# Kernel optimization log

Hardware: AMD Instinct MI355X
Metric: run time of the kernel (lower is better)

The kernel has to match this reference:

```python
import jax, jax.numpy as jnp
import numpy as np
import math

N_STFT = 1025
N_MELS = 128
SAMPLE_RATE = 16000
F_MIN = 0.0
F_MAX = 8000.0
MAX_ITER = 20
LR = 0.3
MOMENTUM = 0.9
BATCH = 4
TIME = 1024


def _create_fb_matrix(n_freqs, f_min, f_max, n_mels, sample_rate):
    # Triangular mel filterbank, (n_freqs, n_mels), matching torchaudio's create_fb_matrix.
    all_freqs = np.linspace(0.0, sample_rate // 2, n_freqs)
    m_min = 2595.0 * math.log10(1.0 + f_min / 700.0)
    m_max = 2595.0 * math.log10(1.0 + f_max / 700.0)
    m_pts = np.linspace(m_min, m_max, n_mels + 2)
    f_pts = 700.0 * (10.0 ** (m_pts / 2595.0) - 1.0)
    f_diff = f_pts[1:] - f_pts[:-1]
    slopes = f_pts[None, :] - all_freqs[:, None]  # (n_freqs, n_mels+2)
    down_slopes = -slopes[:, :-2] / f_diff[:-1]
    up_slopes = slopes[:, 2:] / f_diff[1:]
    fb = np.maximum(0.0, np.minimum(down_slopes, up_slopes))
    return jnp.asarray(fb, dtype=jnp.float32)


def setup_inputs() -> dict:
    key = jax.random.key(0)
    k1, k2 = jax.random.split(key)
    melspec = jax.random.uniform(k1, (BATCH, N_MELS, TIME), dtype=jnp.float32)
    # torch.rand initialization of the estimated spectrogram, exposed for determinism
    spec_init = jax.random.uniform(k2, (BATCH, TIME, N_STFT), dtype=jnp.float32)
    fb = _create_fb_matrix(N_STFT, F_MIN, F_MAX, N_MELS, SAMPLE_RATE)
    return {"melspec": melspec, "spec_init": spec_init, "fb": fb}


def reference(melspec, spec_init, fb):
    # melspec: (B, n_mels, T) -> (B, T, n_mels); fb: (n_stft, n_mels)
    mel_t = jnp.swapaxes(melspec, -1, -2)
    b, t, _ = mel_t.shape
    inv = 2.0 / (b * t)  # d(mean over B*T of sum_m diff^2)/d(spec) prefactor

    def step(carry, _):
        spec, buf = carry
        diff = mel_t - jnp.einsum('btf,fm->btm', spec, fb)      # (B,T,M)
        grad = -inv * jnp.einsum('btm,fm->btf', diff, fb)       # (B,T,F)
        buf = MOMENTUM * buf + grad                              # SGD momentum buffer
        spec = jnp.maximum(spec - LR * buf, 0.0)                 # update + clamp(min=0)
        return (spec, buf), None

    init = (spec_init, jnp.zeros_like(spec_init))
    (spec, _), _ = jax.lax.scan(step, init, None, length=MAX_ITER)
    return jnp.swapaxes(spec, -1, -2)  # (B, n_stft, T)
```

## Files before the change

### kernel.cpp

```cpp
#include <hip/hip_runtime.h>

#define N_STFT 1025
#define N_MELS 128
#define BATCH 4
#define TIME 1024
#define MAX_ITER 20

__global__ void imel_prep(const float* __restrict__ fb, int* __restrict__ m0f,
                          float* __restrict__ w0a, float* __restrict__ w1a) {
  const int w = threadIdx.x >> 6, l = threadIdx.x & 63;
  const int f = blockIdx.x * 4 + w;
  if (f >= N_STFT) return;
  const float* row = fb + (size_t)f * N_MELS;
  const unsigned long long mlo = __ballot(row[l] != 0.0f);
  const unsigned long long mhi = __ballot(row[l + 64] != 0.0f);
  if (l == 0) {
    int m0 = mlo ? __builtin_ctzll(mlo)
                 : (mhi ? 64 + __builtin_ctzll(mhi) : 0);
    if (m0 > N_MELS - 2) m0 = N_MELS - 2;
    m0f[f] = m0;
    w0a[f] = row[m0];
    w1a[f] = row[m0 + 1];
  }
}

__global__ __launch_bounds__(512, 8) void imel_main(
    const float* __restrict__ melspec, const float* __restrict__ spec_init,
    const int* __restrict__ m0f, const float* __restrict__ w0a,
    const float* __restrict__ w1a, float* __restrict__ out) {
  __shared__ int   s_Pi[4][4][129];
  __shared__ float s_diff[4][N_MELS];
  __shared__ float s_out[4][1060];

  const int tid = threadIdx.x;
  const int w   = tid >> 6;
  const int l   = tid & 63;
  const int row = w >> 1;
  const int h   = w & 1;
  const int c   = h * 64 + l;
  const int r   = l & 3;
  const int blk = blockIdx.x;
  const int b   = blk >> 8;
  const int t0  = (blk & 255) << 2;
  const int t   = t0 + row;

  const float SCALE = 16777216.0f;
  const float INV_SCALE = 1.0f / 16777216.0f;

  float rs[9], rb[9], rw0[9], rw1[9];
  int rm0[9];

  const float* srow = spec_init + (size_t)(b * TIME + t) * N_STFT;
#pragma unroll
  for (int k = 0; k < 9; ++k) {
    const int f = (c << 3) + k;
    const bool ok = (k < 8) || (c == 127);
    if (ok) {
      rs[k] = srow[f];
      rm0[k] = m0f[f];
      rw0[k] = w0a[f] * SCALE;
      rw1[k] = w1a[f] * SCALE;
    } else {
      rs[k] = 0.f; rm0[k] = 0; rw0[k] = 0.f; rw1[k] = 0.f;
    }
    rb[k] = 0.f;
  }

  const int dr = tid >> 7, dm = tid & 127;
  const float melD = melspec[((size_t)b * N_MELS + dm) * TIME + t0 + dr];

  for (int i = tid; i < 4 * 4 * 129; i += 512) ((int*)s_Pi)[i] = 0;
  __syncthreads();

  const float GRAD_C = (-2.0f / (BATCH * TIME)) * INV_SCALE;

  for (int it = 0; it < MAX_ITER; ++it) {
#pragma unroll
    for (int k = 0; k < 9; ++k) {
      if (k < 8 || c == 127) {
        atomicAdd(&s_Pi[row][r][rm0[k]],     __float2int_rn(rs[k] * rw0[k]));
        atomicAdd(&s_Pi[row][r][rm0[k] + 1], __float2int_rn(rs[k] * rw1[k]));
      }
    }
    __syncthreads();
    {
      const int p = s_Pi[dr][0][dm] + s_Pi[dr][1][dm] +
                    s_Pi[dr][2][dm] + s_Pi[dr][3][dm];
      s_diff[dr][dm] = melD - (float)p * INV_SCALE;
      s_Pi[dr][0][dm] = 0; s_Pi[dr][1][dm] = 0;
      s_Pi[dr][2][dm] = 0; s_Pi[dr][3][dm] = 0;
    }
    __syncthreads();
#pragma unroll
    for (int k = 0; k < 9; ++k) {
      if (k < 8 || c == 127) {
        const float d0 = s_diff[row][rm0[k]];
        const float d1 = s_diff[row][rm0[k] + 1];
        const float g = GRAD_C * (d0 * rw0[k] + d1 * rw1[k]);
        rb[k] = 0.9f * rb[k] + g;
        const float s = rs[k] - 0.3f * rb[k];
        rs[k] = s > 0.f ? s : 0.f;
      }
    }
  }

#pragma unroll
  for (int k = 0; k < 9; ++k) {
    if (k < 8 || c == 127) {
      const int f = (c << 3) + k;
      s_out[row][f + (f >> 5)] = rs[k];
    }
  }
  __syncthreads();

  const int tl = tid & 3;
  const int fg = tid >> 2;
  float* obase = out + (size_t)b * N_STFT * TIME + t0 + tl;
  for (int f = fg; f < N_STFT; f += 128) {
    obase[(size_t)f * TIME] = s_out[tl][f + (f >> 5)];
  }
}

extern "C" void kernel_launch(void* const* d_in, const int* in_sizes, int n_in,
                              void* d_out, int out_size, void* d_ws, size_t ws_size,
                              hipStream_t stream) {
  const float* melspec = (const float*)d_in[0];
  const float* spec_init = (const float*)d_in[1];
  const float* fb = (const float*)d_in[2];
  float* out = (float*)d_out;

  int* m0f = (int*)d_ws;
  float* w0a = (float*)((char*)d_ws + 5120);
  float* w1a = (float*)((char*)d_ws + 10240);

  imel_prep<<<dim3(257), dim3(256), 0, stream>>>(fb, m0f, w0a, w1a);
  imel_main<<<dim3(1024), dim3(512), 0, stream>>>(melspec, spec_init, m0f, w0a, w1a, out);
}
```

Baseline: 134.4 us.

## Assign one wavefront per time row and combine runs before LDS atomics

Each 64-lane wavefront now owns a whole time row, 16 frequency bins per lane, with a private LDS accumulator. That lets the two block-wide __syncthreads per iteration become wave-level barriers. Bins sharing the same mel index are summed in registers before a single atomic, which cuts LDS atomic traffic. The constant melspec part of the gradient is precomputed once per bin. The last frequency bin is carried through unchanged, which relies on its filterbank row being all zero.

```diff
diff --git a/kernel.cpp b/kernel.cpp
--- a/kernel.cpp
+++ b/kernel.cpp
@@ -5,6 +5,8 @@
 #define BATCH 4
 #define TIME 1024
 #define MAX_ITER 20
+
+typedef unsigned int u32;
 
 __global__ void imel_prep(const float* __restrict__ fb, int* __restrict__ m0f,
                           float* __restrict__ w0a, float* __restrict__ w1a) {
@@ -24,99 +26,107 @@
   }
 }
 
-__global__ __launch_bounds__(512, 8) void imel_main(
+__global__ __launch_bounds__(256, 4) void imel_main(
     const float* __restrict__ melspec, const float* __restrict__ spec_init,
     const int* __restrict__ m0f, const float* __restrict__ w0a,
     const float* __restrict__ w1a, float* __restrict__ out) {
-  __shared__ int   s_Pi[4][4][129];
-  __shared__ float s_diff[4][N_MELS];
+  __shared__ u32   s_P[4][N_MELS];
+  __shared__ float s_mel[4][N_MELS];
   __shared__ float s_out[4][1060];
 
   const int tid = threadIdx.x;
   const int w   = tid >> 6;
   const int l   = tid & 63;
-  const int row = w >> 1;
-  const int h   = w & 1;
-  const int c   = h * 64 + l;
-  const int r   = l & 3;
   const int blk = blockIdx.x;
   const int b   = blk >> 8;
   const int t0  = (blk & 255) << 2;
-  const int t   = t0 + row;
+  const int t   = t0 + w;
 
-  const float SCALE = 16777216.0f;
-  const float INV_SCALE = 1.0f / 16777216.0f;
+  for (int i = tid; i < 4 * N_MELS; i += 256) {
+    const int m = i >> 2, r = i & 3;
+    s_mel[r][m] = melspec[((size_t)b * N_MELS + m) * TIME + t0 + r];
+  }
+  __syncthreads();
 
-  float rs[9], rb[9], rw0[9], rw1[9];
-  int rm0[9];
+  const float SCALE  = 16777216.0f;
+  const float GRAD_N = -2.0f / (BATCH * TIME);
+  const float C2 = (2.0f / (BATCH * TIME)) * 3.5527136788e-15f;
+
+  float rs[16], rb[16], rw0[16], rw1[16], cc[16];
+  int rm[16];
 
   const float* srow = spec_init + (size_t)(b * TIME + t) * N_STFT;
 #pragma unroll
-  for (int k = 0; k < 9; ++k) {
-    const int f = (c << 3) + k;
-    const bool ok = (k < 8) || (c == 127);
-    if (ok) {
-      rs[k] = srow[f];
-      rm0[k] = m0f[f];
-      rw0[k] = w0a[f] * SCALE;
-      rw1[k] = w1a[f] * SCALE;
-    } else {
-      rs[k] = 0.f; rm0[k] = 0; rw0[k] = 0.f; rw1[k] = 0.f;
-    }
-    rb[k] = 0.f;
+  for (int k = 0; k < 16; ++k) {
+    const int f = (l << 4) + k;
+    rs[k] = srow[f];
+    const int m = m0f[f];
+    rm[k] = m;
+    const float w0 = w0a[f], w1 = w1a[f];
+    rw0[k] = w0 * SCALE;
+    rw1[k] = w1 * SCALE;
+    cc[k]  = GRAD_N * fmaf(s_mel[w][m], w0, s_mel[w][m + 1] * w1);
+    rb[k]  = 0.f;
   }
+  const float rtail = (l == 63) ? srow[1024] : 0.f;
 
-  const int dr = tid >> 7, dm = tid & 127;
-  const float melD = melspec[((size_t)b * N_MELS + dm) * TIME + t0 + dr];
+  bool adv[16];
+  adv[0] = false;
+#pragma unroll
+  for (int k = 1; k < 16; ++k) adv[k] = (rm[k] != rm[k - 1]);
 
-  for (int i = tid; i < 4 * 4 * 129; i += 512) ((int*)s_Pi)[i] = 0;
-  __syncthreads();
-
-  const float GRAD_C = (-2.0f / (BATCH * TIME)) * INV_SCALE;
+  u32* __restrict__ Pw = &s_P[w][0];
+  Pw[l] = 0u;
+  Pw[l + 64] = 0u;
 
   for (int it = 0; it < MAX_ITER; ++it) {
+    {
+      float a0 = rs[0] * rw0[0];
+      float a1 = rs[0] * rw1[0];
 #pragma unroll
-    for (int k = 0; k < 9; ++k) {
-      if (k < 8 || c == 127) {
-        atomicAdd(&s_Pi[row][r][rm0[k]],     __float2int_rn(rs[k] * rw0[k]));
-        atomicAdd(&s_Pi[row][r][rm0[k] + 1], __float2int_rn(rs[k] * rw1[k]));
+      for (int k = 1; k < 16; ++k) {
+        if (adv[k]) atomicAdd(&Pw[rm[k - 1]], (u32)__float2int_rn(a0));
+        const float n0 = (adv[k] ? a1 : a0) + rs[k] * rw0[k];
+        a1 = (adv[k] ? 0.f : a1) + rs[k] * rw1[k];
+        a0 = n0;
+      }
+      atomicAdd(&Pw[rm[15]],     (u32)__float2int_rn(a0));
+      atomicAdd(&Pw[rm[15] + 1], (u32)__float2int_rn(a1));
+    }
+    __builtin_amdgcn_wave_barrier();
+    {
+      float p0 = (float)(int)Pw[rm[0]];
+      float p1 = (float)(int)Pw[rm[0] + 1];
+#pragma unroll
+      for (int k = 0; k < 16; ++k) {
+        if (k > 0 && adv[k]) {
+          p0 = p1;
+          p1 = (float)(int)Pw[rm[k] + 1];
+        }
+        const float h = fmaf(p1, rw1[k], p0 * rw0[k]);
+        const float g = fmaf(h, C2, cc[k]);
+        rb[k] = fmaf(0.9f, rb[k], g);
+        rs[k] = fmaxf(fmaf(-0.3f, rb[k], rs[k]), 0.f);
       }
     }
-    __syncthreads();
-    {
-      const int p = s_Pi[dr][0][dm] + s_Pi[dr][1][dm] +
-                    s_Pi[dr][2][dm] + s_Pi[dr][3][dm];
-      s_diff[dr][dm] = melD - (float)p * INV_SCALE;
-      s_Pi[dr][0][dm] = 0; s_Pi[dr][1][dm] = 0;
-      s_Pi[dr][2][dm] = 0; s_Pi[dr][3][dm] = 0;
-    }
-    __syncthreads();
-#pragma unroll
-    for (int k = 0; k < 9; ++k) {
-      if (k < 8 || c == 127) {
-        const float d0 = s_diff[row][rm0[k]];
-        const float d1 = s_diff[row][rm0[k] + 1];
-        const float g = GRAD_C * (d0 * rw0[k] + d1 * rw1[k]);
-        rb[k] = 0.9f * rb[k] + g;
-        const float s = rs[k] - 0.3f * rb[k];
-        rs[k] = s > 0.f ? s : 0.f;
-      }
-    }
+    __builtin_amdgcn_wave_barrier();
+    Pw[l] = 0u;
+    Pw[l + 64] = 0u;
+    __builtin_amdgcn_wave_barrier();
   }
 
 #pragma unroll
-  for (int k = 0; k < 9; ++k) {
-    if (k < 8 || c == 127) {
-      const int f = (c << 3) + k;
-      s_out[row][f + (f >> 5)] = rs[k];
-    }
+  for (int k = 0; k < 16; ++k) {
+    const int f = (l << 4) + k;
+    s_out[w][f + (f >> 5)] = rs[k];
   }
+  if (l == 63) s_out[w][1056] = rtail;
   __syncthreads();
 
   const int tl = tid & 3;
   const int fg = tid >> 2;
   float* obase = out + (size_t)b * N_STFT * TIME + t0 + tl;
-  for (int f = fg; f < N_STFT; f += 128) {
+  for (int f = fg; f < N_STFT; f += 64) {
     obase[(size_t)f * TIME] = s_out[tl][f + (f >> 5)];
   }
 }
@@ -134,5 +144,5 @@
   float* w1a = (float*)((char*)d_ws + 10240);
 
   imel_prep<<<dim3(257), dim3(256), 0, stream>>>(fb, m0f, w0a, w1a);
-  imel_main<<<dim3(1024), dim3(512), 0, stream>>>(melspec, spec_init, m0f, w0a, w1a, out);
+  imel_main<<<dim3(1024), dim3(256), 0, stream>>>(melspec, spec_init, m0f, w0a, w1a, out);
 }
```

After: 133.8 us. About the same (-0.4%).
